# Optimization experiments

Measured on AMD Instinct MI355X. Metric: run time of the kernel, lower is better.

Reference implementation:

```python
import jax, jax.numpy as jnp
import numpy as np

B, T, C = 4, 1024, 768
NH = 12
HD = C // NH  # 64


def setup_inputs() -> dict:
    key = jax.random.key(0)
    k1, k2, k3, k4, k5 = jax.random.split(key, 5)
    s = 0.02
    return {
        "x": jax.random.normal(k1, (B, T, C), dtype=jnp.float32),
        "Wqkv": jax.random.normal(k2, (C, 3 * C), dtype=jnp.float32) * s,
        "bqkv": jax.random.normal(k3, (3 * C,), dtype=jnp.float32) * s,
        "Wproj": jax.random.normal(k4, (C, C), dtype=jnp.float32) * s,
        "bproj": jax.random.normal(k5, (C,), dtype=jnp.float32) * s,
        "start_pos": 0,
    }


def reference(x, Wqkv, bqkv, Wproj, bproj, start_pos):
    # Manual QKV projection (nn.Linear with weight stored as [in, out])
    Bq, Tq, Cq = x.shape
    qkv = x @ Wqkv + bqkv                       # [B, T, 3C]
    q, k, v = jnp.split(qkv, 3, axis=-1)
    q = q.reshape(Bq, Tq, NH, HD)
    k = k.reshape(Bq, Tq, NH, HD)
    v = v.reshape(Bq, Tq, NH, HD)
    # With start_pos=0 the KV-cache write+slice is an identity on k, v.
    att = jnp.einsum("bqhd,bkhd->bhqk", q, k) / jnp.sqrt(jnp.float32(HD))
    causal = jnp.tril(jnp.ones((Tq, Tq), dtype=bool))  # [T, T]
    att = jnp.where(causal[None, None], att, jnp.float32(-jnp.inf))
    att = jax.nn.softmax(att, axis=-1)
    out = jnp.einsum("bhqk,bkhd->bqhd", att, v).reshape(Bq, Tq, Cq)
    return out @ Wproj + bproj
```

## Files before the change

kernel.cpp:

```cpp
#include <hip/hip_runtime.h>


#define BB 4
#define TT 1024
#define CC 768
#define NHH 12
#define HDD 64
#define BHH (BB*NHH)

typedef unsigned short u16;
typedef __attribute__((ext_vector_type(8))) short bf16x8;
typedef __attribute__((ext_vector_type(4))) float f32x4;

__device__ __forceinline__ u16 f2b(float f) {
  unsigned u = __float_as_uint(f);
  u += 0x7fffu + ((u >> 16) & 1u);
  return (u16)(u >> 16);
}
__device__ __forceinline__ u16 f2b_t(float f) {
  return (u16)(__float_as_uint(f) >> 16);
}

__device__ __forceinline__ void gload_lds16(const u16* g, u16* l) {
  __builtin_amdgcn_global_load_lds(
      (const __attribute__((address_space(1))) unsigned int*)g,
      (__attribute__((address_space(3))) unsigned int*)l, 16, 0, 0);
}

__device__ __forceinline__ void tr_body(const float* __restrict__ in, u16* __restrict__ out,
                                        int R, int Cc, int bx, int by, float (*tile)[33]) {
  int c0 = bx * 32, r0 = by * 32;
  int tx = threadIdx.x & 31, ty = threadIdx.x >> 5;
#pragma unroll
  for (int i = 0; i < 32; i += 8)
    tile[ty + i][tx] = in[(r0 + ty + i) * Cc + c0 + tx];
  __syncthreads();
#pragma unroll
  for (int i = 0; i < 32; i += 8)
    out[(c0 + ty + i) * R + r0 + tx] = f2b(tile[tx][ty + i]);
}

__global__ __launch_bounds__(256) void k_prep(const float* __restrict__ x, u16* __restrict__ xb,
                                              const float* __restrict__ Wqkv, u16* __restrict__ Wqkv_t,
                                              const float* __restrict__ Wproj, u16* __restrict__ Wproj_t) {
  __shared__ float tile[32][33];
  int bid = blockIdx.x;
  if (bid < 3072) {
    int i = bid * 256 + threadIdx.x;
    float4 v = ((const float4*)x)[i];
    ushort4 o;
    o.x = f2b(v.x); o.y = f2b(v.y); o.z = f2b(v.z); o.w = f2b(v.w);
    ((ushort4*)xb)[i] = o;
  } else if (bid < 3072 + 1728) {
    int tb = bid - 3072;
    tr_body(Wqkv, Wqkv_t, CC, 3 * CC, tb % 72, tb / 72, tile);
  } else {
    int tb = bid - 4800;
    tr_body(Wproj, Wproj_t, CC, CC, tb % 24, tb / 24, tile);
  }
}

#define GEMM_CORE(A_, Bt_, m0_, n0_, SMEM)                                        \
  u16* As = (SMEM); u16* Bs = (SMEM) + 4096;                                      \
  int tid = threadIdx.x;                                                          \
  int wave = tid >> 6, lane = tid & 63, quad = lane >> 4, id16 = lane & 15;       \
  int wm = (wave & 1) * 64, wn = (wave >> 1) * 64;                                \
  const u16* ga = A_ + (m0_ + (tid >> 2)) * CC + (tid & 3) * 8;                   \
  const u16* gb = Bt_ + (n0_ + (tid >> 2)) * CC + (tid & 3) * 8;                  \
  f32x4 acc[4][4];                                                                \
  _Pragma("unroll") for (int i = 0; i < 4; i++)                                   \
      _Pragma("unroll") for (int j = 0; j < 4; j++) acc[i][j] = (f32x4){0,0,0,0}; \
  for (int k0 = 0; k0 < CC; k0 += 32) {                                           \
    gload_lds16(ga + k0, As + tid * 8);                                           \
    gload_lds16(ga + 64 * CC + k0, As + 64 * 32 + tid * 8);                       \
    gload_lds16(gb + k0, Bs + tid * 8);                                           \
    gload_lds16(gb + 64 * CC + k0, Bs + 64 * 32 + tid * 8);                       \
    __syncthreads();                                                              \
    bf16x8 af[4], bfr[4];                                                         \
    _Pragma("unroll") for (int i = 0; i < 4; i++)                                 \
        af[i] = *(const bf16x8*)(As + (wm + i * 16 + id16) * 32 + quad * 8);      \
    _Pragma("unroll") for (int j = 0; j < 4; j++)                                 \
        bfr[j] = *(const bf16x8*)(Bs + (wn + j * 16 + id16) * 32 + quad * 8);     \
    _Pragma("unroll") for (int i = 0; i < 4; i++)                                 \
        _Pragma("unroll") for (int j = 0; j < 4; j++)                             \
            acc[i][j] = __builtin_amdgcn_mfma_f32_16x16x32_bf16(af[i], bfr[j],    \
                                                                acc[i][j], 0, 0, 0); \
    __syncthreads();                                                              \
  }

__global__ __launch_bounds__(256) void k_qkv(const u16* __restrict__ A, const u16* __restrict__ Bt,
                                             const float* __restrict__ bias,
                                             u16* __restrict__ Qb, u16* __restrict__ Kb,
                                             u16* __restrict__ Vt) {
  __shared__ u16 smem[128 * 136];
  int xcd = blockIdx.x & 7, g = blockIdx.x >> 3;
  int m0 = (xcd + 8 * (g / 18)) * 128, n0 = (g % 18) * 128;
  GEMM_CORE(A, Bt, m0, n0, smem)
  float bv[4];
#pragma unroll
  for (int j = 0; j < 4; j++) bv[j] = bias[n0 + wn + j * 16 + id16];
  int bi = m0 >> 10, t0 = m0 & 1023;

  if (n0 < 2 * CC) {
    u16* dstb = (n0 < CC) ? Qb : Kb;
    int nrel0 = (n0 < CC) ? n0 : n0 - CC;
#pragma unroll
    for (int i = 0; i < 4; i++)
#pragma unroll
      for (int j = 0; j < 4; j++)
#pragma unroll
        for (int r = 0; r < 4; r++)
          smem[(wm + i * 16 + quad * 4 + r) * 136 + wn + j * 16 + id16] =
              f2b(acc[i][j][r] + bv[j]);
    __syncthreads();
    int m_l = tid >> 1, seg = tid & 1;
    int ng = nrel0 + seg * 64;
    u16* dst = dstb + ((bi * NHH + (ng >> 6)) * TT + t0 + m_l) * HDD;
    const u16* src = smem + m_l * 136 + seg * 64;
#pragma unroll
    for (int w2 = 0; w2 < 8; w2++)
      ((bf16x8*)dst)[w2] = ((const bf16x8*)src)[w2];
  } else {
#pragma unroll
    for (int i = 0; i < 4; i++)
#pragma unroll
      for (int j = 0; j < 4; j++)
#pragma unroll
        for (int r = 0; r < 4; r++)
          smem[(wn + j * 16 + id16) * 136 + wm + i * 16 + quad * 4 + r] =
              f2b(acc[i][j][r] + bv[j]);
    __syncthreads();
    int d2 = tid >> 1, seg = tid & 1;
    int h = (n0 - 2 * CC + d2) >> 6;
    int d = d2 & 63;
    u16* dst = Vt + (((bi * NHH + h) * HDD + d) * TT) + t0 + seg * 64;
    const u16* src = smem + d2 * 136 + seg * 64;
#pragma unroll
    for (int w2 = 0; w2 < 8; w2++)
      ((bf16x8*)dst)[w2] = ((const bf16x8*)src)[w2];
  }
}

__global__ __launch_bounds__(256) void k_proj(const u16* __restrict__ A, const u16* __restrict__ Bt,
                                              const float* __restrict__ bias, float* __restrict__ out) {
  __shared__ u16 smem[8192];
  int xcd = blockIdx.x & 7, g = blockIdx.x >> 3;
  int m0 = (xcd + 8 * (g / 6)) * 128, n0 = (g % 6) * 128;
  GEMM_CORE(A, Bt, m0, n0, smem)
  float bv[4];
#pragma unroll
  for (int j = 0; j < 4; j++) bv[j] = bias[n0 + wn + j * 16 + id16];
#pragma unroll
  for (int i = 0; i < 4; i++) {
#pragma unroll
    for (int j = 0; j < 4; j++) {
#pragma unroll
      for (int r = 0; r < 4; r++) {
        int m = m0 + wm + i * 16 + quad * 4 + r;
        int n = n0 + wn + j * 16 + id16;
        out[m * CC + n] = acc[i][j][r] + bv[j];
      }
    }
  }
}

#define PSTR 72
__global__ __launch_bounds__(128) void k_attn(const u16* __restrict__ Qb, const u16* __restrict__ Kb,
                                              const u16* __restrict__ Vt, u16* __restrict__ Ob) {
  __shared__ __align__(16) u16 Ks[2][64 * 64];
  __shared__ __align__(16) u16 Vs[2][64 * 64];
  __shared__ __align__(16) u16 Pl[2][32 * PSTR];
  int tid = threadIdx.x;
  int wave = tid >> 6, lane = tid & 63, quad = lane >> 4, id16 = lane & 15;
  int bh = blockIdx.x % BHH, t = 15 - (blockIdx.x / BHH);
  int b = bh / NHH, h = bh % NHH;
  int qw = t * 64 + wave * 32;
  int nch = t + 1;
  const float cexp = 0.125f * 1.44269504088896f;
  short onev = (id16 == 0) ? (short)0x3F80 : (short)0;
  bf16x8 bones = {onev, onev, onev, onev, onev, onev, onev, onev};

  const u16* Kg = Kb + (bh * TT) * HDD;
  const u16* Vg = Vt + (bh * HDD) * TT;
  int srow = tid >> 3, spart = tid & 7;

  bf16x8 aq[2][2];
#pragma unroll
  for (int rh = 0; rh < 2; rh++) {
    const u16* Qrow = Qb + (bh * TT + qw + 16 * rh + id16) * HDD;
    aq[rh][0] = *(const bf16x8*)(Qrow + quad * 8);
    aq[rh][1] = *(const bf16x8*)(Qrow + 32 + quad * 8);
  }
  f32x4 o[2][4], ol[2];
#pragma unroll
  for (int rh = 0; rh < 2; rh++) {
    ol[rh] = (f32x4){0,0,0,0};
#pragma unroll
    for (int dt = 0; dt < 4; dt++) o[rh][dt] = (f32x4){0,0,0,0};
  }

#pragma unroll
  for (int i = 0; i < 4; i++) {
    gload_lds16(Kg + (16 * i + srow) * HDD + spart * 8, Ks[0] + i * 1024 + tid * 8);
    gload_lds16(Vg + (16 * i + srow) * TT + spart * 8, Vs[0] + i * 1024 + tid * 8);
  }

  for (int c = 0; c < nch; c++) {
    __syncthreads();
    if (c + 1 < nch) {
      int kb = (c + 1) * 64;
      u16* kd = Ks[(c + 1) & 1];
      u16* vd = Vs[(c + 1) & 1];
#pragma unroll
      for (int i = 0; i < 4; i++) {
        gload_lds16(Kg + (kb + 16 * i + srow) * HDD + spart * 8, kd + i * 1024 + tid * 8);
        gload_lds16(Vg + (16 * i + srow) * TT + kb + spart * 8, vd + i * 1024 + tid * 8);
      }
    }
    const u16* kbuf = Ks[c & 1];
    const u16* vbuf = Vs[c & 1];

    bf16x8 kf0[4], kf1[4];
#pragma unroll
    for (int kt = 0; kt < 4; kt++) {
      kf0[kt] = *(const bf16x8*)(kbuf + (kt * 16 + id16) * 64 + quad * 8);
      kf1[kt] = *(const bf16x8*)(kbuf + (kt * 16 + id16) * 64 + 32 + quad * 8);
    }

    u16* Pb = Pl[wave];
    bool diag = (c == nch - 1);
#pragma unroll
    for (int rh = 0; rh < 2; rh++) {
      f32x4 s[4];
#pragma unroll
      for (int kt = 0; kt < 4; kt++) {
        f32x4 z = {0,0,0,0};
        z = __builtin_amdgcn_mfma_f32_16x16x32_bf16(aq[rh][0], kf0[kt], z, 0, 0, 0);
        s[kt] = __builtin_amdgcn_mfma_f32_16x16x32_bf16(aq[rh][1], kf1[kt], z, 0, 0, 0);
      }
      if (!diag) {
#pragma unroll
        for (int kt = 0; kt < 4; kt++)
#pragma unroll
          for (int r = 0; r < 4; r++)
            Pb[(16 * rh + quad * 4 + r) * PSTR + kt * 16 + id16] =
                f2b_t(__builtin_amdgcn_exp2f(s[kt][r] * cexp));
      } else {
        int kb = c * 64;
#pragma unroll
        for (int kt = 0; kt < 4; kt++) {
          int col = kb + kt * 16 + id16;
#pragma unroll
          for (int r = 0; r < 4; r++) {
            float p = __builtin_amdgcn_exp2f(s[kt][r] * cexp);
            p = (col <= qw + 16 * rh + quad * 4 + r) ? p : 0.f;
            Pb[(16 * rh + quad * 4 + r) * PSTR + kt * 16 + id16] = f2b_t(p);
          }
        }
      }
    }
    asm volatile("s_waitcnt lgkmcnt(0)" ::: "memory");

    bf16x8 pf[2][2];
#pragma unroll
    for (int rh = 0; rh < 2; rh++) {
      pf[rh][0] = *(const bf16x8*)(Pb + (16 * rh + id16) * PSTR + quad * 8);
      pf[rh][1] = *(const bf16x8*)(Pb + (16 * rh + id16) * PSTR + 32 + quad * 8);
    }
#pragma unroll
    for (int dt = 0; dt < 4; dt++) {
      bf16x8 vf0 = *(const bf16x8*)(vbuf + (dt * 16 + id16) * 64 + quad * 8);
      bf16x8 vf1 = *(const bf16x8*)(vbuf + (dt * 16 + id16) * 64 + 32 + quad * 8);
#pragma unroll
      for (int rh = 0; rh < 2; rh++) {
        o[rh][dt] = __builtin_amdgcn_mfma_f32_16x16x32_bf16(pf[rh][0], vf0, o[rh][dt], 0, 0, 0);
        o[rh][dt] = __builtin_amdgcn_mfma_f32_16x16x32_bf16(pf[rh][1], vf1, o[rh][dt], 0, 0, 0);
      }
    }
#pragma unroll
    for (int rh = 0; rh < 2; rh++) {
      ol[rh] = __builtin_amdgcn_mfma_f32_16x16x32_bf16(pf[rh][0], bones, ol[rh], 0, 0, 0);
      ol[rh] = __builtin_amdgcn_mfma_f32_16x16x32_bf16(pf[rh][1], bones, ol[rh], 0, 0, 0);
    }
  }

#pragma unroll
  for (int rh = 0; rh < 2; rh++) {
    int outbase = (b * TT + qw + 16 * rh + quad * 4) * CC + h * HDD;
#pragma unroll
    for (int r = 0; r < 4; r++) {
      float l = __shfl(ol[rh][r], 0, 16);
      float inv = 1.0f / l;
      Ob[outbase + r * CC + id16]      = f2b(o[rh][0][r] * inv);
      Ob[outbase + r * CC + 16 + id16] = f2b(o[rh][1][r] * inv);
      Ob[outbase + r * CC + 32 + id16] = f2b(o[rh][2][r] * inv);
      Ob[outbase + r * CC + 48 + id16] = f2b(o[rh][3][r] * inv);
    }
  }
}

extern "C" void kernel_launch(void* const* d_in, const int* in_sizes, int n_in,
                              void* d_out, int out_size, void* d_ws, size_t ws_size,
                              hipStream_t stream) {
  const float* x     = (const float*)d_in[0];
  const float* Wqkv  = (const float*)d_in[1];
  const float* bqkv  = (const float*)d_in[2];
  const float* Wproj = (const float*)d_in[3];
  const float* bproj = (const float*)d_in[4];
  float* out = (float*)d_out;

  u16* ws = (u16*)d_ws;
  u16* xb      = ws;
  u16* Wqkv_t  = xb + BB * TT * CC;
  u16* Wproj_t = Wqkv_t + 3 * CC * CC;
  u16* Qb      = Wproj_t + CC * CC;
  u16* Kb      = Qb + BHH * TT * HDD;
  u16* Vt      = Kb + BHH * TT * HDD;
  u16* Ob      = Vt + BHH * TT * HDD;

  k_prep<<<3072 + 1728 + 576, 256, 0, stream>>>(x, xb, Wqkv, Wqkv_t, Wproj, Wproj_t);
  k_qkv<<<32 * 18, 256, 0, stream>>>(xb, Wqkv_t, bqkv, Qb, Kb, Vt);
  k_attn<<<16 * BHH, 128, 0, stream>>>(Qb, Kb, Vt, Ob);
  k_proj<<<32 * 6, 256, 0, stream>>>(Ob, Wproj_t, bproj, out);
}
```

Baseline: 161.9 us.

## Keep attention probabilities in registers by computing transposed S^T

The attention kernel now computes S^T by swapping the MFMA operands, so each lane's exp'd probability outputs already match the B-operand layout of the PV MFMA. This removes the per-wave LDS staging buffer for P, the lgkmcnt wait and the LDS read-back. V fragments are gathered with 4-element loads permuted to the matching k ordering. The output is produced transposed (O^T), so each lane now writes 4 packed bf16 values per store. The cost is extra V register usage and more, smaller LDS reads for V.

```diff
diff --git a/kernel.cpp b/kernel.cpp
--- a/kernel.cpp
+++ b/kernel.cpp
@@ -10,15 +10,17 @@
 
 typedef unsigned short u16;
 typedef __attribute__((ext_vector_type(8))) short bf16x8;
+typedef __attribute__((ext_vector_type(4))) short bf16x4;
 typedef __attribute__((ext_vector_type(4))) float f32x4;
+typedef __attribute__((ext_vector_type(4))) int i32x4;
 
 __device__ __forceinline__ u16 f2b(float f) {
   unsigned u = __float_as_uint(f);
   u += 0x7fffu + ((u >> 16) & 1u);
   return (u16)(u >> 16);
 }
-__device__ __forceinline__ u16 f2b_t(float f) {
-  return (u16)(__float_as_uint(f) >> 16);
+__device__ __forceinline__ unsigned packbf(float lo, float hi) {
+  return (__float_as_uint(hi) & 0xffff0000u) | (__float_as_uint(lo) >> 16);
 }
 
 __device__ __forceinline__ void gload_lds16(const u16* g, u16* l) {
@@ -164,12 +166,10 @@
   }
 }
 
-#define PSTR 72
 __global__ __launch_bounds__(128) void k_attn(const u16* __restrict__ Qb, const u16* __restrict__ Kb,
                                               const u16* __restrict__ Vt, u16* __restrict__ Ob) {
   __shared__ __align__(16) u16 Ks[2][64 * 64];
   __shared__ __align__(16) u16 Vs[2][64 * 64];
-  __shared__ __align__(16) u16 Pl[2][32 * PSTR];
   int tid = threadIdx.x;
   int wave = tid >> 6, lane = tid & 63, quad = lane >> 4, id16 = lane & 15;
   int bh = blockIdx.x % BHH, t = 15 - (blockIdx.x / BHH);
@@ -177,8 +177,9 @@
   int qw = t * 64 + wave * 32;
   int nch = t + 1;
   const float cexp = 0.125f * 1.44269504088896f;
-  short onev = (id16 == 0) ? (short)0x3F80 : (short)0;
-  bf16x8 bones = {onev, onev, onev, onev, onev, onev, onev, onev};
+  bf16x8 bones;
+#pragma unroll
+  for (int e = 0; e < 8; e++) bones[e] = (short)0x3F80;
 
   const u16* Kg = Kb + (bh * TT) * HDD;
   const u16* Vg = Vt + (bh * HDD) * TT;
@@ -219,6 +220,8 @@
     }
     const u16* kbuf = Ks[c & 1];
     const u16* vbuf = Vs[c & 1];
+    bool diag = (c == nch - 1);
+    int kb = c * 64;
 
     bf16x8 kf0[4], kf1[4];
 #pragma unroll
@@ -226,75 +229,83 @@
       kf0[kt] = *(const bf16x8*)(kbuf + (kt * 16 + id16) * 64 + quad * 8);
       kf1[kt] = *(const bf16x8*)(kbuf + (kt * 16 + id16) * 64 + 32 + quad * 8);
     }
-
-    u16* Pb = Pl[wave];
-    bool diag = (c == nch - 1);
+    bf16x8 vf0[4], vf1[4];
+#pragma unroll
+    for (int dt = 0; dt < 4; dt++) {
+      const u16* vr = vbuf + (dt * 16 + id16) * 64;
+      bf16x4 a0 = *(const bf16x4*)(vr + quad * 4);
+      bf16x4 a1 = *(const bf16x4*)(vr + 16 + quad * 4);
+      bf16x4 a2 = *(const bf16x4*)(vr + 32 + quad * 4);
+      bf16x4 a3 = *(const bf16x4*)(vr + 48 + quad * 4);
+#pragma unroll
+      for (int e = 0; e < 4; e++) {
+        vf0[dt][e] = a0[e]; vf0[dt][4 + e] = a1[e];
+        vf1[dt][e] = a2[e]; vf1[dt][4 + e] = a3[e];
+      }
+    }
+
 #pragma unroll
     for (int rh = 0; rh < 2; rh++) {
-      f32x4 s[4];
+      f32x4 st[4];
 #pragma unroll
       for (int kt = 0; kt < 4; kt++) {
         f32x4 z = {0,0,0,0};
-        z = __builtin_amdgcn_mfma_f32_16x16x32_bf16(aq[rh][0], kf0[kt], z, 0, 0, 0);
-        s[kt] = __builtin_amdgcn_mfma_f32_16x16x32_bf16(aq[rh][1], kf1[kt], z, 0, 0, 0);
-      }
+        z = __builtin_amdgcn_mfma_f32_16x16x32_bf16(kf0[kt], aq[rh][0], z, 0, 0, 0);
+        st[kt] = __builtin_amdgcn_mfma_f32_16x16x32_bf16(kf1[kt], aq[rh][1], z, 0, 0, 0);
+      }
+      unsigned pk[4][2];
       if (!diag) {
 #pragma unroll
-        for (int kt = 0; kt < 4; kt++)
-#pragma unroll
-          for (int r = 0; r < 4; r++)
-            Pb[(16 * rh + quad * 4 + r) * PSTR + kt * 16 + id16] =
-                f2b_t(__builtin_amdgcn_exp2f(s[kt][r] * cexp));
+        for (int kt = 0; kt < 4; kt++) {
+          pk[kt][0] = packbf(__builtin_amdgcn_exp2f(st[kt][0] * cexp),
+                             __builtin_amdgcn_exp2f(st[kt][1] * cexp));
+          pk[kt][1] = packbf(__builtin_amdgcn_exp2f(st[kt][2] * cexp),
+                             __builtin_amdgcn_exp2f(st[kt][3] * cexp));
+        }
       } else {
-        int kb = c * 64;
+        int qrow = qw + 16 * rh + id16;
 #pragma unroll
         for (int kt = 0; kt < 4; kt++) {
-          int col = kb + kt * 16 + id16;
+          float pv[4];
 #pragma unroll
           for (int r = 0; r < 4; r++) {
-            float p = __builtin_amdgcn_exp2f(s[kt][r] * cexp);
-            p = (col <= qw + 16 * rh + quad * 4 + r) ? p : 0.f;
-            Pb[(16 * rh + quad * 4 + r) * PSTR + kt * 16 + id16] = f2b_t(p);
+            int key = kb + kt * 16 + quad * 4 + r;
+            float p = __builtin_amdgcn_exp2f(st[kt][r] * cexp);
+            pv[r] = (key <= qrow) ? p : 0.f;
           }
+          pk[kt][0] = packbf(pv[0], pv[1]);
+          pk[kt][1] = packbf(pv[2], pv[3]);
         }
       }
-    }
-    asm volatile("s_waitcnt lgkmcnt(0)" ::: "memory");
-
-    bf16x8 pf[2][2];
-#pragma unroll
-    for (int rh = 0; rh < 2; rh++) {
-      pf[rh][0] = *(const bf16x8*)(Pb + (16 * rh + id16) * PSTR + quad * 8);
-      pf[rh][1] = *(const bf16x8*)(Pb + (16 * rh + id16) * PSTR + 32 + quad * 8);
-    }
+      i32x4 b0v, b1v;
+      b0v.x = (int)pk[0][0]; b0v.y = (int)pk[0][1];
+      b0v.z = (int)pk[1][0]; b0v.w = (int)pk[1][1];
+      b1v.x = (int)pk[2][0]; b1v.y = (int)pk[2][1];
+      b1v.z = (int)pk[3][0]; b1v.w = (int)pk[3][1];
+      bf16x8 pf0 = __builtin_bit_cast(bf16x8, b0v);
+      bf16x8 pf1 = __builtin_bit_cast(bf16x8, b1v);
+
+#pragma unroll
+      for (int dt = 0; dt < 4; dt++) {
+        o[rh][dt] = __builtin_amdgcn_mfma_f32_16x16x32_bf16(vf0[dt], pf0, o[rh][dt], 0, 0, 0);
+        o[rh][dt] = __builtin_amdgcn_mfma_f32_16x16x32_bf16(vf1[dt], pf1, o[rh][dt], 0, 0, 0);
+      }
+      ol[rh] = __builtin_amdgcn_mfma_f32_16x16x32_bf16(bones, pf0, ol[rh], 0, 0, 0);
+      ol[rh] = __builtin_amdgcn_mfma_f32_16x16x32_bf16(bones, pf1, ol[rh], 0, 0, 0);
+    }
+  }
+
+#pragma unroll
+  for (int rh = 0; rh < 2; rh++) {
+    float inv = 1.0f / ol[rh][0];
+    int qg = qw + 16 * rh + id16;
+    u16* dst = Ob + (b * TT + qg) * CC + h * HDD + quad * 4;
 #pragma unroll
     for (int dt = 0; dt < 4; dt++) {
-      bf16x8 vf0 = *(const bf16x8*)(vbuf + (dt * 16 + id16) * 64 + quad * 8);
-      bf16x8 vf1 = *(const bf16x8*)(vbuf + (dt * 16 + id16) * 64 + 32 + quad * 8);
-#pragma unroll
-      for (int rh = 0; rh < 2; rh++) {
-        o[rh][dt] = __builtin_amdgcn_mfma_f32_16x16x32_bf16(pf[rh][0], vf0, o[rh][dt], 0, 0, 0);
-        o[rh][dt] = __builtin_amdgcn_mfma_f32_16x16x32_bf16(pf[rh][1], vf1, o[rh][dt], 0, 0, 0);
-      }
-    }
-#pragma unroll
-    for (int rh = 0; rh < 2; rh++) {
-      ol[rh] = __builtin_amdgcn_mfma_f32_16x16x32_bf16(pf[rh][0], bones, ol[rh], 0, 0, 0);
-      ol[rh] = __builtin_amdgcn_mfma_f32_16x16x32_bf16(pf[rh][1], bones, ol[rh], 0, 0, 0);
-    }
-  }
-
-#pragma unroll
-  for (int rh = 0; rh < 2; rh++) {
-    int outbase = (b * TT + qw + 16 * rh + quad * 4) * CC + h * HDD;
-#pragma unroll
-    for (int r = 0; r < 4; r++) {
-      float l = __shfl(ol[rh][r], 0, 16);
-      float inv = 1.0f / l;
-      Ob[outbase + r * CC + id16]      = f2b(o[rh][0][r] * inv);
-      Ob[outbase + r * CC + 16 + id16] = f2b(o[rh][1][r] * inv);
-      Ob[outbase + r * CC + 32 + id16] = f2b(o[rh][2][r] * inv);
-      Ob[outbase + r * CC + 48 + id16] = f2b(o[rh][3][r] * inv);
+      unsigned lo = ((unsigned)f2b(o[rh][dt][1] * inv) << 16) | f2b(o[rh][dt][0] * inv);
+      unsigned hi = ((unsigned)f2b(o[rh][dt][3] * inv) << 16) | f2b(o[rh][dt][2] * inv);
+      uint2 pairv; pairv.x = lo; pairv.y = hi;
+      *(uint2*)(dst + dt * 16) = pairv;
     }
   }
 }
```

Measured after the change: 175.3 us. 1.08x slower.
